# Performance work log

Measured on AMD Instinct MI355X. Metric: run time of the kernel, lower is better.

Reference implementation:

```python
import jax, jax.numpy as jnp
import numpy as np

B, R, C, E, H = 2, 16, 512, 1024, 16
D = E // H  # head_dim = 64


def setup_inputs() -> dict:
    key = jax.random.key(0)
    ks = jax.random.split(key, 9)
    s = 1.0 / np.sqrt(E)
    return {
        "x": jax.random.normal(ks[0], (B, R, C, E), dtype=jnp.float32),
        "wq": jax.random.uniform(ks[1], (E, E), jnp.float32, -s, s),
        "bq": jax.random.uniform(ks[2], (E,), jnp.float32, -s, s),
        "wk": jax.random.uniform(ks[3], (E, E), jnp.float32, -s, s),
        "bk": jax.random.uniform(ks[4], (E,), jnp.float32, -s, s),
        "wv": jax.random.uniform(ks[5], (E, E), jnp.float32, -s, s),
        "bv": jax.random.uniform(ks[6], (E,), jnp.float32, -s, s),
        "wo": jax.random.uniform(ks[7], (E, E), jnp.float32, -s, s),
        "bo": jax.random.uniform(ks[8], (E,), jnp.float32, -s, s),
    }


def reference(x, wq, bq, wk, bk, wv, bv, wo, bo):
    b, r, c, e = x.shape
    # projections: [b,r,c,e] -> [b,r,h,c,d]
    def split_heads(t):
        return t.reshape(b, r, c, H, D).transpose(0, 1, 3, 2, 4)
    q = split_heads(x @ wq + bq)
    k = split_heads(x @ wk + bk)
    v = split_heads(x @ wv + bv)
    scale = 1.0 / jnp.sqrt(jnp.asarray(D, x.dtype))
    logits = jnp.einsum('brhqd,brhkd->brhqk', q, k) * scale
    probs = jax.nn.softmax(logits, axis=-1)
    ctx = jnp.einsum('brhqk,brhkd->brhqd', probs, v)
    ctx = ctx.transpose(0, 1, 3, 2, 4).reshape(b, r, c, e)
    return ctx @ wo + bo
```

## Files before the change

kernel.cpp:

```cpp
#include <hip/hip_runtime.h>
#include <hip/hip_bf16.h>
#include <hip/hip_fp16.h>
#include <math.h>

typedef _Float16 half8 __attribute__((ext_vector_type(8)));
typedef __attribute__((ext_vector_type(4))) float floatx4;

constexpr int Bc = 2, Rc = 16, Cc = 512, Ec = 1024, Hc = 16, Dc = 64;
#define QSCALE 0.180336880111120425f

__device__ inline void gl_lds16(const void* g, void* l) {
  __builtin_amdgcn_global_load_lds(
      (const __attribute__((address_space(1))) void*)g,
      (__attribute__((address_space(3))) void*)l, 16, 0, 0);
}
__device__ inline unsigned short f2h(float f) {
  __half h = __float2half_rn(f);
  return *(unsigned short*)&h;
}
__device__ inline unsigned int pack_h2(float lo, float hi) {
  __half2 p = __float22half2_rn(make_float2(lo, hi));
  return *(unsigned int*)&p;
}

__global__ __launch_bounds__(256) void cvt_x(const float* __restrict__ x,
                                             unsigned short* __restrict__ xh) {
  const size_t base = ((size_t)blockIdx.x * 256 + threadIdx.x) * 8;
  float4 a = *(const float4*)(x + base);
  float4 b = *(const float4*)(x + base + 4);
  uint4 o;
  o.x = pack_h2(a.x, a.y);
  o.y = pack_h2(a.z, a.w);
  o.z = pack_h2(b.x, b.y);
  o.w = pack_h2(b.z, b.w);
  *(uint4*)(xh + base) = o;
}

__global__ __launch_bounds__(256) void wprep(
    const float* __restrict__ w0, const float* __restrict__ w1,
    const float* __restrict__ w2, const float* __restrict__ w3,
    unsigned short* __restrict__ t0, unsigned short* __restrict__ t1,
    unsigned short* __restrict__ t2, unsigned short* __restrict__ t3) {
  __shared__ float tile[64][65];
  const int z = blockIdx.z;
  const float* W = (z == 0) ? w0 : (z == 1) ? w1 : (z == 2) ? w2 : w3;
  unsigned short* T = (z == 0) ? t0 : (z == 1) ? t1 : (z == 2) ? t2 : t3;
  const int tid = threadIdx.x;
  const int bk = blockIdx.x * 64, bn = blockIdx.y * 64;
#pragma unroll
  for (int p = 0; p < 16; ++p) {
    int idx = p * 256 + tid;
    int lk = idx >> 6, ln = idx & 63;
    tile[ln][lk] = W[(size_t)(bk + lk) * 1024 + bn + ln];
  }
  __syncthreads();
#pragma unroll
  for (int p = 0; p < 16; ++p) {
    int idx = p * 256 + tid;
    int ln = idx >> 6, lk = idx & 63;
    T[(size_t)(bn + ln) * 1024 + bk + lk] = f2h(tile[ln][lk]);
  }
}

#define WAIT_VM(N)                                                            \
  {                                                                           \
    asm volatile("s_waitcnt vmcnt(" #N ")" ::: "memory");                     \
    __builtin_amdgcn_sched_barrier(0);                                        \
  }

#define STG_AB(SBUF, KT)                                                      \
  {                                                                           \
    _Pragma("unroll") for (int l_ = 0; l_ < 2; ++l_) {                        \
      const int r0_ = l_ * 128 + w * 16;                                      \
      gl_lds16(Ab + (size_t)r0_ * 1024 + glan + (size_t)(KT) * 32,            \
               As + (SBUF) * 8192 + r0_ * 32);                                \
      gl_lds16(Bb + (size_t)r0_ * 1024 + glan + (size_t)(KT) * 32,            \
               Bs + (SBUF) * 8192 + r0_ * 32);                                \
    }                                                                         \
  }

#define DSR(NBUF, FA, FB)                                                     \
  {                                                                           \
    _Pragma("unroll") for (int i_ = 0; i_ < 8; ++i_) FA[i_] =                 \
        *(const half8*)&As[(NBUF) * 8192 + (wm + i_ * 16 + lr) * 32 + qk];    \
    _Pragma("unroll") for (int j_ = 0; j_ < 4; ++j_) FB[j_] =                 \
        *(const half8*)&Bs[(NBUF) * 8192 + (wn + j_ * 16 + lr) * 32 + qk];    \
  }

#define MFMA32(FA, FB)                                                        \
  _Pragma("unroll") for (int i_ = 0; i_ < 8; ++i_)                            \
      _Pragma("unroll") for (int j_ = 0; j_ < 4; ++j_) acc[i_][j_] =          \
          __builtin_amdgcn_mfma_f32_16x16x32_f16(FA[i_], FB[j_],              \
                                                 acc[i_][j_], 0, 0, 0);

#define TSTEP(NBUF, SBUF, KT, FA, FB, NFA, NFB, STGE, NXTE, VMW)              \
  {                                                                           \
    if (STGE) STG_AB(SBUF, KT);                                               \
    if (NXTE) DSR(NBUF, NFA, NFB);                                            \
    MFMA32(FA, FB);                                                           \
    if ((VMW) == 1) { WAIT_VM(4); }                                           \
    if ((VMW) == 2) { WAIT_VM(0); }                                           \
    if ((VMW) != 3) {                                                         \
      __builtin_amdgcn_s_barrier();                                           \
      __builtin_amdgcn_sched_barrier(0);                                      \
    }                                                                         \
  }

template <int MODE>
__global__ __launch_bounds__(512, 2) void gemm256(
    const unsigned short* __restrict__ gA, const unsigned short* __restrict__ gB,
    const float* __restrict__ bq, const float* __restrict__ bk,
    const float* __restrict__ bv, unsigned short* __restrict__ qout,
    unsigned short* __restrict__ kout, unsigned short* __restrict__ vout,
    float* __restrict__ fout, const float* __restrict__ bo) {
  __shared__ unsigned short As[4 * 8192];
  __shared__ unsigned short Bs[4 * 8192];
  const int tid = threadIdx.x;
  const int w = tid >> 6, ln = tid & 63;
  const int lr = ln & 15, quad = ln >> 4;
  const int qk = quad * 8;
  const int wm = (w >> 2) * 128, wn = (w & 3) * 64;
  int bm, bn;
  if (MODE == 0) {
    const int swz = (blockIdx.x & 7) * 96 + (blockIdx.x >> 3);
    bm = (swz / 12) * 256;
    bn = (swz % 12) * 256;
  } else {
    const int swz = (blockIdx.x & 7) * 32 + (blockIdx.x >> 3);
    bm = (swz >> 2) * 256;
    bn = (swz & 3) * 256;
  }
  const unsigned short* Ab = gA + (size_t)bm * 1024;
  const unsigned short* Bb = gB + (size_t)bn * 1024;
  const int glan = (ln >> 2) * 1024 + (ln & 3) * 8;

  floatx4 acc[8][4];
#pragma unroll
  for (int i = 0; i < 8; ++i)
#pragma unroll
    for (int j = 0; j < 4; ++j) acc[i][j] = (floatx4)(0.f);
  half8 fa0[8], fb0[4], fa1[8], fb1[4];

  STG_AB(0, 0);
  STG_AB(1, 1);
  STG_AB(2, 2);
  WAIT_VM(4);
  __builtin_amdgcn_s_barrier();
  __builtin_amdgcn_sched_barrier(0);
  DSR(0, fa0, fb0);

  for (int tt = 0; tt < 7; ++tt) {
    const int k4 = tt * 4;
    TSTEP(1, 3, k4 + 3, fa0, fb0, fa1, fb1, 1, 1, 1);
    TSTEP(2, 0, k4 + 4, fa1, fb1, fa0, fb0, 1, 1, 1);
    TSTEP(3, 1, k4 + 5, fa0, fb0, fa1, fb1, 1, 1, 1);
    TSTEP(0, 2, k4 + 6, fa1, fb1, fa0, fb0, 1, 1, 1);
  }
  TSTEP(1, 3, 31, fa0, fb0, fa1, fb1, 1, 1, 1);
  TSTEP(2, 0, 0, fa1, fb1, fa0, fb0, 0, 1, 2);
  TSTEP(3, 0, 0, fa0, fb0, fa1, fb1, 0, 1, 3);
  TSTEP(0, 0, 0, fa1, fb1, fa0, fb0, 0, 0, 3);

  const int q4 = quad * 4;
  const bool odd = ln & 1;
  if constexpr (MODE == 0) {
    const int z = bn >> 10;
    const float* bias = (z == 0) ? bq : (z == 1) ? bk : bv;
    const int czb = (bn & 1023) + wn;
#pragma unroll
    for (int i = 0; i < 8; ++i) {
#pragma unroll
      for (int j = 0; j < 4; ++j) {
        const int colz = czb + j * 16 + lr;
        float v[4];
#pragma unroll
        for (int r = 0; r < 4; ++r) v[r] = acc[i][j][r] + bias[colz];
        const int m0 = bm + wm + i * 16 + q4;
        const int h = colz >> 6, d = colz & 63;
        const int brr = m0 >> 9, c0 = m0 & 511;
        const size_t hb = ((size_t)brr * 16 + h) * 32768;
        if (z == 2) {
          uint2 o;
          o.x = pack_h2(v[0], v[1]);
          o.y = pack_h2(v[2], v[3]);
          *(uint2*)(vout + hb + (size_t)d * 512 + c0) = o;
        } else {
          unsigned short* outp = (z == 0) ? qout : kout;
          if (z == 0) {
#pragma unroll
            for (int r = 0; r < 4; ++r) v[r] *= QSCALE;
          }
#pragma unroll
          for (int rp = 0; rp < 2; ++rp) {
            float a = v[2 * rp], b = v[2 * rp + 1];
            float ax = __shfl_xor(a, 1), bx = __shfl_xor(b, 1);
            unsigned int u = odd ? pack_h2(bx, b) : pack_h2(a, ax);
            const int c = c0 + 2 * rp + (odd ? 1 : 0);
            const int dd = d & ~1;
            *(unsigned int*)(outp + hb + (size_t)c * 64 + dd) = u;
          }
        }
      }
    }
  } else {
#pragma unroll
    for (int i = 0; i < 8; ++i)
#pragma unroll
      for (int j = 0; j < 4; ++j) {
        const int col = bn + wn + j * 16 + lr;
#pragma unroll
        for (int r = 0; r < 4; ++r) {
          const int m = bm + wm + i * 16 + q4 + r;
          fout[(size_t)m * 1024 + col] = acc[i][j][r] + bo[col];
        }
      }
  }
}

__global__ __launch_bounds__(256, 2) void attn_mfma(
    const unsigned short* __restrict__ Qh, const unsigned short* __restrict__ Kb,
    const unsigned short* __restrict__ Vt, unsigned short* __restrict__ Ctx) {
  __shared__ unsigned short Ks[128 * 64];
  __shared__ unsigned short Vs[64 * 128];
  __shared__ unsigned short Ps[128][136];

  const int t = threadIdx.x;
  const int w = t >> 6, ln = t & 63;
  const int lane15 = ln & 15, quad = ln >> 4;
  const bool odd = ln & 1;
  const int bh = blockIdx.x >> 2;
  const int qb = (blockIdx.x & 3) * 128;

  half8 qf[2][2];
  {
    const size_t qbase =
        ((size_t)bh * 512 + qb + w * 32 + lane15) * 64 + quad * 8;
#pragma unroll
    for (int i = 0; i < 2; ++i)
#pragma unroll
      for (int c = 0; c < 2; ++c)
        qf[i][c] = *(const half8*)(Qh + qbase + (size_t)i * 16 * 64 + c * 32);
  }

  floatx4 oacc[2][4];
#pragma unroll
  for (int i = 0; i < 2; ++i)
#pragma unroll
    for (int dj = 0; dj < 4; ++dj) oacc[i][dj] = (floatx4)(0.f);
  float lsum[2][4];
#pragma unroll
  for (int i = 0; i < 2; ++i)
#pragma unroll
    for (int r = 0; r < 4; ++r) lsum[i][r] = 0.f;

  const unsigned short* kgb = Kb + (size_t)bh * 32768;
  const unsigned short* vgb = Vt + (size_t)bh * 32768;

  for (int kt = 0; kt < 512; kt += 128) {
    __syncthreads();
    {
      const unsigned short* kq = kgb + (size_t)kt * 64;
#pragma unroll
      for (int p = 0; p < 4; ++p) {
        const int s = p * 256 + t;
        const int kr = s >> 3, kc16 = s & 7;
        gl_lds16(kq + kr * 64 + ((kc16 ^ (kr & 7)) << 3), (char*)Ks + s * 16);
        const int vr = s >> 4, vc16 = s & 15;
        gl_lds16(vgb + vr * 512 + kt + ((vc16 ^ (vr & 15)) << 3),
                 (char*)Vs + s * 16);
      }
    }
    __syncthreads();

    floatx4 sacc[2][8];
#pragma unroll
    for (int i = 0; i < 2; ++i)
#pragma unroll
      for (int j = 0; j < 8; ++j) sacc[i][j] = (floatx4)(0.f);
#pragma unroll
    for (int j = 0; j < 8; ++j) {
      const int krow = j * 16 + lane15;
      const unsigned short* kr = Ks + krow * 64;
      half8 kf0 = *(const half8*)(kr + ((quad ^ (krow & 7)) << 3));
      half8 kf1 = *(const half8*)(kr + (((4 + quad) ^ (krow & 7)) << 3));
#pragma unroll
      for (int i = 0; i < 2; ++i) {
        sacc[i][j] = __builtin_amdgcn_mfma_f32_16x16x32_f16(qf[i][0], kf0,
                                                            sacc[i][j], 0, 0, 0);
        sacc[i][j] = __builtin_amdgcn_mfma_f32_16x16x32_f16(qf[i][1], kf1,
                                                            sacc[i][j], 0, 0, 0);
      }
    }

#pragma unroll
    for (int i = 0; i < 2; ++i) {
#pragma unroll
      for (int rp = 0; rp < 2; ++rp) {
        const int rA = rp * 2, rB = rA + 1;
        const int row = w * 32 + i * 16 + quad * 4 + rA + (odd ? 1 : 0);
        unsigned short* prow = &Ps[row][lane15 & ~1];
#pragma unroll
        for (int j = 0; j < 8; ++j) {
          const float pA = exp2f(sacc[i][j][rA]);
          const float pB = exp2f(sacc[i][j][rB]);
          lsum[i][rA] += pA;
          lsum[i][rB] += pB;
          const float an = __shfl_xor(pA, 1);
          const float bn = __shfl_xor(pB, 1);
          const float lo = odd ? bn : pA;
          const float hi = odd ? pB : an;
          *(unsigned int*)(prow + j * 16) = pack_h2(lo, hi);
        }
      }
    }

#pragma unroll
    for (int kc = 0; kc < 4; ++kc) {
      half8 pa0 = *(const half8*)&Ps[w * 32 + lane15][kc * 32 + quad * 8];
      half8 pa1 = *(const half8*)&Ps[w * 32 + 16 + lane15][kc * 32 + quad * 8];
#pragma unroll
      for (int dj = 0; dj < 4; ++dj) {
        const int drow = dj * 16 + lane15;
        half8 vf = *(const half8*)(
            Vs + drow * 128 + (((kc * 4 + quad) ^ (drow & 15)) << 3));
        oacc[0][dj] = __builtin_amdgcn_mfma_f32_16x16x32_f16(pa0, vf,
                                                             oacc[0][dj], 0, 0, 0);
        oacc[1][dj] = __builtin_amdgcn_mfma_f32_16x16x32_f16(pa1, vf,
                                                             oacc[1][dj], 0, 0, 0);
      }
    }
  }

  float invl[2][4];
#pragma unroll
  for (int i = 0; i < 2; ++i)
#pragma unroll
    for (int r = 0; r < 4; ++r) {
      float ls = lsum[i][r];
#pragma unroll
      for (int off = 1; off < 16; off <<= 1) ls += __shfl_xor(ls, off);
      invl[i][r] = 1.f / ls;
    }
  const int br = bh >> 4, h = bh & 15;
  const size_t mbase = (size_t)br * 512 + qb + w * 32;
#pragma unroll
  for (int i = 0; i < 2; ++i)
#pragma unroll
    for (int dj = 0; dj < 4; ++dj) {
      const int e = h * 64 + dj * 16 + lane15;
      const int ee = e & ~1;
#pragma unroll
      for (int rp = 0; rp < 2; ++rp) {
        const int rA = 2 * rp, rB = rA + 1;
        float a = oacc[i][dj][rA] * invl[i][rA];
        float b = oacc[i][dj][rB] * invl[i][rB];
        float ax = __shfl_xor(a, 1), bx = __shfl_xor(b, 1);
        unsigned int u = odd ? pack_h2(bx, b) : pack_h2(a, ax);
        const size_t m = mbase + i * 16 + quad * 4 + rA + (odd ? 1 : 0);
        *(unsigned int*)(Ctx + m * 1024 + ee) = u;
      }
    }
}

extern "C" void kernel_launch(void* const* d_in, const int* in_sizes, int n_in,
                              void* d_out, int out_size, void* d_ws,
                              size_t ws_size, hipStream_t stream) {
  const float* x = (const float*)d_in[0];
  const float* wq = (const float*)d_in[1];
  const float* bq = (const float*)d_in[2];
  const float* wk = (const float*)d_in[3];
  const float* bk = (const float*)d_in[4];
  const float* wv = (const float*)d_in[5];
  const float* bv = (const float*)d_in[6];
  const float* wo = (const float*)d_in[7];
  const float* bo = (const float*)d_in[8];
  float* out = (float*)d_out;

  char* w = (char*)d_ws;
  const size_t MiB = 1ull << 20;
  unsigned short* qbuf = (unsigned short*)(w + 0 * MiB);
  unsigned short* kbuf = (unsigned short*)(w + 32 * MiB);
  unsigned short* vtb = (unsigned short*)(w + 64 * MiB);
  unsigned short* xh = (unsigned short*)(w + 96 * MiB);
  unsigned short* ctx = (unsigned short*)(w + 128 * MiB);
  unsigned short* wqh = (unsigned short*)(w + 160 * MiB);
  unsigned short* wkh = (unsigned short*)(w + 162 * MiB);
  unsigned short* wvh = (unsigned short*)(w + 164 * MiB);
  unsigned short* woh = (unsigned short*)(w + 166 * MiB);

  cvt_x<<<8192, 256, 0, stream>>>(x, xh);
  wprep<<<dim3(16, 16, 4), 256, 0, stream>>>(wq, wk, wv, wo, wqh, wkh, wvh,
                                             woh);

  gemm256<0><<<768, 512, 0, stream>>>(xh, wqh, bq, bk, bv, qbuf, kbuf, vtb,
                                      nullptr, nullptr);

  attn_mfma<<<2048, 256, 0, stream>>>(qbuf, kbuf, vtb, ctx);

  gemm256<1><<<256, 512, 0, stream>>>(ctx, woh, nullptr, nullptr, nullptr,
                                      nullptr, nullptr, nullptr, out, bo);
}
```

Baseline: 394.3 us.

## Load B fragments directly from pre-swizzled global layout; XOR-swizzle A in LDS

The weight-prep kernel now writes the transposed fp16 weights in an MFMA-fragment-ordered layout, so the GEMM loads B operands straight from global memory into registers and no longer stages them through LDS. The A tile gets an XOR swizzle on both the global-to-LDS store and the LDS read to cut bank conflicts. The waitcnt/barrier schedule is reworked and s_setprio is wrapped around the MFMA block. This halves LDS traffic and footprint, but every wave now issues its own global loads for B, which leans on L2 reuse and adds register pressure.

```diff
diff --git a/kernel.cpp b/kernel.cpp
--- a/kernel.cpp
+++ b/kernel.cpp
@@ -50,42 +50,52 @@
 #pragma unroll
   for (int p = 0; p < 16; ++p) {
     int idx = p * 256 + tid;
-    int lk = idx >> 6, ln = idx & 63;
-    tile[ln][lk] = W[(size_t)(bk + lk) * 1024 + bn + ln];
+    int lk = idx >> 6, lnn = idx & 63;
+    tile[lnn][lk] = W[(size_t)(bk + lk) * 1024 + bn + lnn];
   }
   __syncthreads();
-#pragma unroll
-  for (int p = 0; p < 16; ++p) {
-    int idx = p * 256 + tid;
-    int ln = idx >> 6, lk = idx & 63;
-    T[(size_t)(bn + ln) * 1024 + bk + lk] = f2h(tile[ln][lk]);
+  const int lane = tid & 63, sub = tid >> 6;
+  const int lr = lane & 15, quad = lane >> 4;
+#pragma unroll
+  for (int tl = 0; tl < 2; ++tl) {
+    float v[8];
+#pragma unroll
+    for (int jj = 0; jj < 8; ++jj)
+      v[jj] = tile[sub * 16 + lr][tl * 32 + quad * 8 + jj];
+    uint4 o;
+    o.x = pack_h2(v[0], v[1]);
+    o.y = pack_h2(v[2], v[3]);
+    o.z = pack_h2(v[4], v[5]);
+    o.w = pack_h2(v[6], v[7]);
+    const size_t n16 = (size_t)(bn >> 4) + sub;
+    const size_t tt = (size_t)(bk >> 5) + tl;
+    *(uint4*)(T + ((n16 * 32 + tt) * 64 + lane) * 8) = o;
   }
 }
 
 #define WAIT_VM(N)                                                            \
   {                                                                           \
+    __builtin_amdgcn_sched_barrier(0);                                        \
     asm volatile("s_waitcnt vmcnt(" #N ")" ::: "memory");                     \
     __builtin_amdgcn_sched_barrier(0);                                        \
   }
 
-#define STG_AB(SBUF, KT)                                                      \
+#define STG_A(SBUF, KT)                                                       \
   {                                                                           \
     _Pragma("unroll") for (int l_ = 0; l_ < 2; ++l_) {                        \
       const int r0_ = l_ * 128 + w * 16;                                      \
       gl_lds16(Ab + (size_t)r0_ * 1024 + glan + (size_t)(KT) * 32,            \
                As + (SBUF) * 8192 + r0_ * 32);                                \
-      gl_lds16(Bb + (size_t)r0_ * 1024 + glan + (size_t)(KT) * 32,            \
-               Bs + (SBUF) * 8192 + r0_ * 32);                                \
     }                                                                         \
   }
 
-#define DSR(NBUF, FA, FB)                                                     \
-  {                                                                           \
-    _Pragma("unroll") for (int i_ = 0; i_ < 8; ++i_) FA[i_] =                 \
-        *(const half8*)&As[(NBUF) * 8192 + (wm + i_ * 16 + lr) * 32 + qk];    \
-    _Pragma("unroll") for (int j_ = 0; j_ < 4; ++j_) FB[j_] =                 \
-        *(const half8*)&Bs[(NBUF) * 8192 + (wn + j_ * 16 + lr) * 32 + qk];    \
-  }
+#define BLOAD(FB, KT)                                                         \
+  _Pragma("unroll") for (int j_ = 0; j_ < 4; ++j_) FB[j_] =                   \
+      *(const half8*)(Bf + bqoff + (size_t)j_ * 16384 + (size_t)(KT) * 512);
+
+#define DSRA(NBUF, FA)                                                        \
+  _Pragma("unroll") for (int i_ = 0; i_ < 8; ++i_) FA[i_] =                   \
+      *(const half8*)&As[(NBUF) * 8192 + (wm + i_ * 16 + lr) * 32 + swq];
 
 #define MFMA32(FA, FB)                                                        \
   _Pragma("unroll") for (int i_ = 0; i_ < 8; ++i_)                            \
@@ -93,14 +103,17 @@
           __builtin_amdgcn_mfma_f32_16x16x32_f16(FA[i_], FB[j_],              \
                                                  acc[i_][j_], 0, 0, 0);
 
-#define TSTEP(NBUF, SBUF, KT, FA, FB, NFA, NFB, STGE, NXTE, VMW)              \
+#define TSTEP(NBUF, SBUF, KSTG, KBLD, FA, FB, NFA, NFB, STGE, BLDE, DSRE,     \
+              VMN, BARE)                                                      \
   {                                                                           \
-    if (STGE) STG_AB(SBUF, KT);                                               \
-    if (NXTE) DSR(NBUF, NFA, NFB);                                            \
+    if (STGE) STG_A(SBUF, KSTG);                                              \
+    if (BLDE) BLOAD(NFB, KBLD);                                               \
+    if (DSRE) DSRA(NBUF, NFA);                                                \
+    WAIT_VM(VMN);                                                             \
+    __builtin_amdgcn_s_setprio(1);                                            \
     MFMA32(FA, FB);                                                           \
-    if ((VMW) == 1) { WAIT_VM(4); }                                           \
-    if ((VMW) == 2) { WAIT_VM(0); }                                           \
-    if ((VMW) != 3) {                                                         \
+    __builtin_amdgcn_s_setprio(0);                                            \
+    if (BARE) {                                                               \
       __builtin_amdgcn_s_barrier();                                           \
       __builtin_amdgcn_sched_barrier(0);                                      \
     }                                                                         \
@@ -114,11 +127,9 @@
     unsigned short* __restrict__ kout, unsigned short* __restrict__ vout,
     float* __restrict__ fout, const float* __restrict__ bo) {
   __shared__ unsigned short As[4 * 8192];
-  __shared__ unsigned short Bs[4 * 8192];
   const int tid = threadIdx.x;
   const int w = tid >> 6, ln = tid & 63;
   const int lr = ln & 15, quad = ln >> 4;
-  const int qk = quad * 8;
   const int wm = (w >> 2) * 128, wn = (w & 3) * 64;
   int bm, bn;
   if (MODE == 0) {
@@ -131,35 +142,39 @@
     bn = (swz & 3) * 256;
   }
   const unsigned short* Ab = gA + (size_t)bm * 1024;
-  const unsigned short* Bb = gB + (size_t)bn * 1024;
-  const int glan = (ln >> 2) * 1024 + (ln & 3) * 8;
+  const unsigned short* Bf = gB;
+  const size_t bqoff =
+      (size_t)((bn >> 4) + (w & 3) * 4) * 16384 + (size_t)ln * 8;
+  const int glan = (ln >> 2) * 1024 + (((ln & 3) ^ ((ln >> 3) & 3)) << 3);
+  const int swq = ((quad ^ ((lr >> 1) & 3)) << 3);
 
   floatx4 acc[8][4];
 #pragma unroll
   for (int i = 0; i < 8; ++i)
 #pragma unroll
     for (int j = 0; j < 4; ++j) acc[i][j] = (floatx4)(0.f);
-  half8 fa0[8], fb0[4], fa1[8], fb1[4];
-
-  STG_AB(0, 0);
-  STG_AB(1, 1);
-  STG_AB(2, 2);
-  WAIT_VM(4);
+  half8 fa0[8], fa1[8], fb0[4], fb1[4];
+
+  STG_A(0, 0);
+  STG_A(1, 1);
+  STG_A(2, 2);
+  BLOAD(fb0, 0);
+  WAIT_VM(6);
   __builtin_amdgcn_s_barrier();
   __builtin_amdgcn_sched_barrier(0);
-  DSR(0, fa0, fb0);
+  DSRA(0, fa0);
 
   for (int tt = 0; tt < 7; ++tt) {
     const int k4 = tt * 4;
-    TSTEP(1, 3, k4 + 3, fa0, fb0, fa1, fb1, 1, 1, 1);
-    TSTEP(2, 0, k4 + 4, fa1, fb1, fa0, fb0, 1, 1, 1);
-    TSTEP(3, 1, k4 + 5, fa0, fb0, fa1, fb1, 1, 1, 1);
-    TSTEP(0, 2, k4 + 6, fa1, fb1, fa0, fb0, 1, 1, 1);
-  }
-  TSTEP(1, 3, 31, fa0, fb0, fa1, fb1, 1, 1, 1);
-  TSTEP(2, 0, 0, fa1, fb1, fa0, fb0, 0, 1, 2);
-  TSTEP(3, 0, 0, fa0, fb0, fa1, fb1, 0, 1, 3);
-  TSTEP(0, 0, 0, fa1, fb1, fa0, fb0, 0, 0, 3);
+    TSTEP(1, 3, k4 + 3, k4 + 1, fa0, fb0, fa1, fb1, 1, 1, 1, 6, 1);
+    TSTEP(2, 0, k4 + 4, k4 + 2, fa1, fb1, fa0, fb0, 1, 1, 1, 6, 1);
+    TSTEP(3, 1, k4 + 5, k4 + 3, fa0, fb0, fa1, fb1, 1, 1, 1, 6, 1);
+    TSTEP(0, 2, k4 + 6, k4 + 4, fa1, fb1, fa0, fb0, 1, 1, 1, 6, 1);
+  }
+  TSTEP(1, 3, 31, 29, fa0, fb0, fa1, fb1, 1, 1, 1, 6, 1);
+  TSTEP(2, 0, 0, 30, fa1, fb1, fa0, fb0, 0, 1, 1, 4, 1);
+  TSTEP(3, 0, 0, 31, fa0, fb0, fa1, fb1, 0, 1, 1, 4, 1);
+  TSTEP(0, 0, 0, 0, fa1, fb1, fa0, fb0, 0, 0, 0, 0, 0);
 
   const int q4 = quad * 4;
   const bool odd = ln & 1;
```

Result: faster. 371.8 us (-5.7%).
